# Performance work log

Hardware: AMD Instinct MI355X
Metric: run time of the kernel (lower is better)

Reference implementation:

```python
import jax, jax.numpy as jnp
import numpy as np
import math

B, N, C = 4096, 64, 128
H = 4
HD = C // H


def setup_inputs() -> dict:
    key = jax.random.key(0)
    ks = jax.random.split(key, 8)
    s = 1.0 / math.sqrt(C)
    return {
        "x": jax.random.normal(ks[0], (B, N, C), dtype=jnp.float32),
        "entropy_map": jax.random.uniform(ks[1], (B, 1, N), dtype=jnp.float32),
        "Wq": jax.random.normal(ks[2], (C, C), dtype=jnp.float32) * s,
        "bq": jnp.zeros((C,), dtype=jnp.float32),
        "Wk": jax.random.normal(ks[3], (C, C), dtype=jnp.float32) * s,
        "bk": jnp.zeros((C,), dtype=jnp.float32),
        "Wv": jax.random.normal(ks[4], (C, C), dtype=jnp.float32) * s,
        "bv": jnp.zeros((C,), dtype=jnp.float32),
        "Wo": jax.random.normal(ks[5], (C, C), dtype=jnp.float32) * s,
        "bo": jnp.zeros((C,), dtype=jnp.float32),
        "beta": 1,
    }


def reference(x, entropy_map, Wq, bq, Wk, bk, Wv, bv, Wo, bo, beta):
    b, n, c = x.shape
    # torch Linear: y = x @ W^T + b
    def proj(w, bias):
        y = jnp.einsum("bnc,dc->bnd", x, w) + bias
        return y.reshape(b, n, H, HD).transpose(0, 2, 1, 3)  # (B,H,N,HD)

    Q = proj(Wq, bq)
    K = proj(Wk, bk)
    V = proj(Wv, bv)
    scale = 1.0 / math.sqrt(HD)
    scores = jnp.einsum("bhnd,bhmd->bhnm", Q, K) * scale  # (B,H,N,N)
    attn = jax.nn.softmax(scores, axis=-1)
    # entropy gating: (B,1,N) -> (B,1,1,N), scales key columns then renormalizes
    gating = jnp.exp(-beta * entropy_map)[:, None, :, :]
    attn = attn * gating
    attn = attn / (attn.sum(axis=-1, keepdims=True) + 1e-9)
    out = jnp.einsum("bhnm,bhmd->bhnd", attn, V)  # (B,H,N,HD)
    out = out.transpose(0, 2, 1, 3).reshape(b, n, c)
    return jnp.einsum("bnc,dc->bnd", out, Wo) + bo
```

## Files before the change

### kernel.cpp

```cpp
#include <hip/hip_runtime.h>
#include <hip/hip_bf16.h>

#define NTOK 64
#define CDIM 128

typedef __attribute__((ext_vector_type(4))) float  f32x4;
typedef __attribute__((ext_vector_type(8))) short  bf16x8;
typedef __attribute__((ext_vector_type(4))) short  s16x4;

__device__ __forceinline__ short f2bf(float f) {
  unsigned u = __float_as_uint(f);
  unsigned r = (u + 0x7fffu + ((u >> 16) & 1u)) >> 16;
  return (short)r;
}

__device__ __forceinline__ int swz(int row, int cb, int stride) {
  return row * stride + (cb ^ ((row & 7) << 4));
}

__global__ void wconv_kernel(const float* __restrict__ wq, const float* __restrict__ wk,
                             const float* __restrict__ wv, const float* __restrict__ wo,
                             short* __restrict__ wbf) {
  int t = blockIdx.x * 256 + threadIdx.x;
  wbf[t]         = f2bf(wq[t]);
  wbf[16384 + t] = f2bf(wk[t]);
  wbf[32768 + t] = f2bf(wv[t]);
  wbf[49152 + t] = f2bf(wo[t]);
}

#define XO_OFF   0
#define Q_OFF    16384
#define K_OFF    32768
#define P_OFF    16384
#define VT_OFF   49152
#define GATE_OFF 65536
#define SMEM_BYTES (65536 + 256)

__global__ __launch_bounds__(256, 2) void fused_attn(
    const float* __restrict__ x, const float* __restrict__ ent,
    const short* __restrict__ wbf,
    const float* __restrict__ bq, const float* __restrict__ bk,
    const float* __restrict__ bv, const float* __restrict__ bo,
    const int* __restrict__ beta, float* __restrict__ out)
{
  __shared__ unsigned char sm[SMEM_BYTES];
  float* gate = (float*)(sm + GATE_OFF);
  const int tid  = threadIdx.x;
  const int lane = tid & 63;
  const int w    = tid >> 6;
  const int g    = lane >> 4;
  const int li   = lane & 15;
  const int b    = blockIdx.x;

  {
    const float* xb = x + (size_t)b * (NTOK * CDIM);
    #pragma unroll
    for (int it = 0; it < 8; ++it) {
      int f = (tid + 256 * it) * 4;
      int row = f >> 7, col = f & 127;
      float4 v = *reinterpret_cast<const float4*>(xb + f);
      s16x4 pk;
      pk.x = f2bf(v.x); pk.y = f2bf(v.y); pk.z = f2bf(v.z); pk.w = f2bf(v.w);
      *reinterpret_cast<s16x4*>(sm + XO_OFF + swz(row, col * 2, 256)) = pk;
    }
    if (tid < NTOK) {
      float bf = (float)beta[0];
      gate[tid] = -bf * ent[(size_t)b * NTOK + tid];
    }
  }
  __syncthreads();

  bf16x8 xf[4][4];
  #pragma unroll
  for (int ti = 0; ti < 4; ++ti) {
    #pragma unroll
    for (int kk = 0; kk < 4; ++kk) {
      int row = ti * 16 + li;
      int cb  = (kk * 32 + g * 8) * 2;
      xf[ti][kk] = *reinterpret_cast<const bf16x8*>(sm + XO_OFF + swz(row, cb, 256));
    }
  }

  const f32x4 zero4 = {0.f, 0.f, 0.f, 0.f};

  {
    const short* wmat = wbf + ((w < 2) ? 0 : 16384);
    const float* bias = (w < 2) ? bq : bk;
    const int dbase   = (w & 1) * 64;
    const int qkbase  = (w < 2) ? Q_OFF : K_OFF;

    f32x4 acc[4][4];
    #pragma unroll
    for (int mi = 0; mi < 4; ++mi)
      #pragma unroll
      for (int ni = 0; ni < 4; ++ni) acc[mi][ni] = zero4;

    #pragma unroll
    for (int mi = 0; mi < 4; ++mi) {
      bf16x8 af[4];
      #pragma unroll
      for (int kk = 0; kk < 4; ++kk)
        af[kk] = *reinterpret_cast<const bf16x8*>(wmat + (dbase + mi * 16 + li) * CDIM + kk * 32 + g * 8);
      #pragma unroll
      for (int ni = 0; ni < 4; ++ni)
        #pragma unroll
        for (int kk = 0; kk < 4; ++kk)
          acc[mi][ni] = __builtin_amdgcn_mfma_f32_16x16x32_bf16(af[kk], xf[ni][kk], acc[mi][ni], 0, 0, 0);
    }
    #pragma unroll
    for (int mi = 0; mi < 4; ++mi) {
      int d0 = dbase + mi * 16 + g * 4;
      float b0 = bias[d0 + 0], b1 = bias[d0 + 1], b2 = bias[d0 + 2], b3 = bias[d0 + 3];
      #pragma unroll
      for (int ni = 0; ni < 4; ++ni) {
        int row = ni * 16 + li;
        int cb  = d0 * 2;
        s16x4 pk;
        pk.x = f2bf(acc[mi][ni].x + b0);
        pk.y = f2bf(acc[mi][ni].y + b1);
        pk.z = f2bf(acc[mi][ni].z + b2);
        pk.w = f2bf(acc[mi][ni].w + b3);
        *reinterpret_cast<s16x4*>(sm + qkbase + swz(row, cb, 256)) = pk;
      }
    }
  }

  {
    const short* wv_ = wbf + 32768;
    f32x4 accv[4][2];
    #pragma unroll
    for (int mi = 0; mi < 4; ++mi) { accv[mi][0] = zero4; accv[mi][1] = zero4; }
    bf16x8 bfv[2][4];
    #pragma unroll
    for (int n2 = 0; n2 < 2; ++n2)
      #pragma unroll
      for (int kk = 0; kk < 4; ++kk)
        bfv[n2][kk] = *reinterpret_cast<const bf16x8*>(wv_ + (w * 32 + n2 * 16 + li) * CDIM + kk * 32 + g * 8);
    #pragma unroll
    for (int mi = 0; mi < 4; ++mi)
      #pragma unroll
      for (int n2 = 0; n2 < 2; ++n2)
        #pragma unroll
        for (int kk = 0; kk < 4; ++kk)
          accv[mi][n2] = __builtin_amdgcn_mfma_f32_16x16x32_bf16(xf[mi][kk], bfv[n2][kk], accv[mi][n2], 0, 0, 0);
    #pragma unroll
    for (int mi = 0; mi < 4; ++mi) {
      #pragma unroll
      for (int n2 = 0; n2 < 2; ++n2) {
        int d = w * 32 + n2 * 16 + li;
        float bb = bv[d];
        int cb = (mi * 16 + g * 4) * 2;
        s16x4 pk;
        pk.x = f2bf(accv[mi][n2].x + bb);
        pk.y = f2bf(accv[mi][n2].y + bb);
        pk.z = f2bf(accv[mi][n2].z + bb);
        pk.w = f2bf(accv[mi][n2].w + bb);
        *reinterpret_cast<s16x4*>(sm + VT_OFF + swz(d, cb, 128)) = pk;
      }
    }
  }
  __syncthreads();

  const float scale = 0.17677669529663688f;
  f32x4 st[4][4];
  {
    bf16x8 kf[4], qf[4];
    int cb = (w * 32 + g * 8) * 2;
    #pragma unroll
    for (int t = 0; t < 4; ++t) {
      int row = t * 16 + li;
      kf[t] = *reinterpret_cast<const bf16x8*>(sm + K_OFF + swz(row, cb, 256));
      qf[t] = *reinterpret_cast<const bf16x8*>(sm + Q_OFF + swz(row, cb, 256));
    }
    #pragma unroll
    for (int mj = 0; mj < 4; ++mj)
      #pragma unroll
      for (int ni = 0; ni < 4; ++ni)
        st[mj][ni] = __builtin_amdgcn_mfma_f32_16x16x32_bf16(kf[mj], qf[ni], zero4, 0, 0, 0);
  }
  float gv[16];
  #pragma unroll
  for (int mj = 0; mj < 4; ++mj)
    #pragma unroll
    for (int r = 0; r < 4; ++r)
      gv[mj * 4 + r] = gate[mj * 16 + g * 4 + r];

  #pragma unroll
  for (int ni = 0; ni < 4; ++ni) {
    float mx = -3.0e38f;
    #pragma unroll
    for (int mj = 0; mj < 4; ++mj) {
      f32x4 v = st[mj][ni];
      v.x = v.x * scale + gv[mj * 4 + 0];
      v.y = v.y * scale + gv[mj * 4 + 1];
      v.z = v.z * scale + gv[mj * 4 + 2];
      v.w = v.w * scale + gv[mj * 4 + 3];
      st[mj][ni] = v;
      mx = fmaxf(mx, fmaxf(fmaxf(v.x, v.y), fmaxf(v.z, v.w)));
    }
    mx = fmaxf(mx, __shfl_xor(mx, 16));
    mx = fmaxf(mx, __shfl_xor(mx, 32));
    float sum = 0.f;
    #pragma unroll
    for (int mj = 0; mj < 4; ++mj) {
      f32x4 v = st[mj][ni];
      v.x = __expf(v.x - mx); v.y = __expf(v.y - mx);
      v.z = __expf(v.z - mx); v.w = __expf(v.w - mx);
      st[mj][ni] = v;
      sum += v.x + v.y + v.z + v.w;
    }
    sum += __shfl_xor(sum, 16);
    sum += __shfl_xor(sum, 32);
    float inv = 1.f / (sum + 1e-9f);
    #pragma unroll
    for (int mj = 0; mj < 4; ++mj) {
      st[mj][ni].x *= inv; st[mj][ni].y *= inv;
      st[mj][ni].z *= inv; st[mj][ni].w *= inv;
    }
  }
  __syncthreads();

  const int pb = P_OFF + w * 8192;
  #pragma unroll
  for (int mj = 0; mj < 4; ++mj) {
    int cb = (mj * 16 + g * 4) * 2;
    #pragma unroll
    for (int ni = 0; ni < 4; ++ni) {
      int row = ni * 16 + li;
      s16x4 pk;
      pk.x = f2bf(st[mj][ni].x); pk.y = f2bf(st[mj][ni].y);
      pk.z = f2bf(st[mj][ni].z); pk.w = f2bf(st[mj][ni].w);
      *reinterpret_cast<s16x4*>(sm + pb + swz(row, cb, 128)) = pk;
    }
  }

  {
    f32x4 accO[2][4];
    #pragma unroll
    for (int md = 0; md < 2; ++md)
      #pragma unroll
      for (int ni = 0; ni < 4; ++ni) accO[md][ni] = zero4;
    bf16x8 vf[2][2];
    #pragma unroll
    for (int md = 0; md < 2; ++md)
      #pragma unroll
      for (int ks = 0; ks < 2; ++ks) {
        int row = w * 32 + md * 16 + li;
        int cb  = (ks * 32 + g * 8) * 2;
        vf[md][ks] = *reinterpret_cast<const bf16x8*>(sm + VT_OFF + swz(row, cb, 128));
      }
    bf16x8 pf[4][2];
    #pragma unroll
    for (int ni = 0; ni < 4; ++ni)
      #pragma unroll
      for (int ks = 0; ks < 2; ++ks) {
        int row = ni * 16 + li;
        int cb  = (ks * 32 + g * 8) * 2;
        pf[ni][ks] = *reinterpret_cast<const bf16x8*>(sm + pb + swz(row, cb, 128));
      }
    #pragma unroll
    for (int md = 0; md < 2; ++md)
      #pragma unroll
      for (int ni = 0; ni < 4; ++ni)
        #pragma unroll
        for (int ks = 0; ks < 2; ++ks)
          accO[md][ni] = __builtin_amdgcn_mfma_f32_16x16x32_bf16(vf[md][ks], pf[ni][ks], accO[md][ni], 0, 0, 0);
    #pragma unroll
    for (int md = 0; md < 2; ++md) {
      int cb = (w * 32 + md * 16 + g * 4) * 2;
      #pragma unroll
      for (int ni = 0; ni < 4; ++ni) {
        int row = ni * 16 + li;
        s16x4 pk;
        pk.x = f2bf(accO[md][ni].x); pk.y = f2bf(accO[md][ni].y);
        pk.z = f2bf(accO[md][ni].z); pk.w = f2bf(accO[md][ni].w);
        *reinterpret_cast<s16x4*>(sm + XO_OFF + swz(row, cb, 256)) = pk;
      }
    }
  }
  __syncthreads();

  {
    const short* wo_ = wbf + 49152;
    f32x4 accY[4][2];
    #pragma unroll
    for (int mi = 0; mi < 4; ++mi) { accY[mi][0] = zero4; accY[mi][1] = zero4; }
    bf16x8 of[4][4];
    #pragma unroll
    for (int mi = 0; mi < 4; ++mi)
      #pragma unroll
      for (int kk = 0; kk < 4; ++kk) {
        int row = mi * 16 + li;
        int cb  = (kk * 32 + g * 8) * 2;
        of[mi][kk] = *reinterpret_cast<const bf16x8*>(sm + XO_OFF + swz(row, cb, 256));
      }
    bf16x8 wf[2][4];
    #pragma unroll
    for (int n2 = 0; n2 < 2; ++n2)
      #pragma unroll
      for (int kk = 0; kk < 4; ++kk)
        wf[n2][kk] = *reinterpret_cast<const bf16x8*>(wo_ + (w * 32 + n2 * 16 + li) * CDIM + kk * 32 + g * 8);
    #pragma unroll
    for (int mi = 0; mi < 4; ++mi)
      #pragma unroll
      for (int n2 = 0; n2 < 2; ++n2)
        #pragma unroll
        for (int kk = 0; kk < 4; ++kk)
          accY[mi][n2] = __builtin_amdgcn_mfma_f32_16x16x32_bf16(of[mi][kk], wf[n2][kk], accY[mi][n2], 0, 0, 0);
    float* yb = out + (size_t)b * (NTOK * CDIM);
    #pragma unroll
    for (int n2 = 0; n2 < 2; ++n2) {
      int dout = w * 32 + n2 * 16 + li;
      float bb = bo[dout];
      #pragma unroll
      for (int mi = 0; mi < 4; ++mi) {
        int i0 = mi * 16 + g * 4;
        yb[(i0 + 0) * CDIM + dout] = accY[mi][n2].x + bb;
        yb[(i0 + 1) * CDIM + dout] = accY[mi][n2].y + bb;
        yb[(i0 + 2) * CDIM + dout] = accY[mi][n2].z + bb;
        yb[(i0 + 3) * CDIM + dout] = accY[mi][n2].w + bb;
      }
    }
  }
}

extern "C" void kernel_launch(void* const* d_in, const int* in_sizes, int n_in,
                              void* d_out, int out_size, void* d_ws, size_t ws_size,
                              hipStream_t stream) {
  const float* x    = (const float*)d_in[0];
  const float* ent  = (const float*)d_in[1];
  const float* wq   = (const float*)d_in[2];
  const float* bq   = (const float*)d_in[3];
  const float* wk   = (const float*)d_in[4];
  const float* bk   = (const float*)d_in[5];
  const float* wv   = (const float*)d_in[6];
  const float* bv   = (const float*)d_in[7];
  const float* wo   = (const float*)d_in[8];
  const float* bo   = (const float*)d_in[9];
  const int*   beta = (const int*)d_in[10];

  short* wbf = (short*)d_ws;
  const int B = in_sizes[0] / (NTOK * CDIM);

  wconv_kernel<<<64, 256, 0, stream>>>(wq, wk, wv, wo, wbf);
  fused_attn<<<B, 256, 0, stream>>>(x, ent, wbf, bq, bk, bv, bo, beta, (float*)d_out);
}
```

Measured before the change: 108.1 us.

## Shrink shared memory to 48KB for three blocks per CU and vectorize output stores

Reorders the projections so V is computed before Q/K, which lets Q overwrite the x buffer and the P and attention-output buffers reuse the freed regions. Shared memory drops from 64KB to 48KB, and launch bounds are raised to three blocks per CU to increase occupancy. It also swaps operands in the output projection so each thread writes contiguous float4 values, replaces the manual bf16 rounding with packed conversion intrinsics, and vectorizes the weight conversion kernel. The extra barriers needed for buffer reuse and the tighter register budget could offset the occupancy gain.

```diff
diff --git a/kernel.cpp b/kernel.cpp
--- a/kernel.cpp
+++ b/kernel.cpp
@@ -8,10 +8,11 @@
 typedef __attribute__((ext_vector_type(8))) short  bf16x8;
 typedef __attribute__((ext_vector_type(4))) short  s16x4;
 
-__device__ __forceinline__ short f2bf(float f) {
-  unsigned u = __float_as_uint(f);
-  unsigned r = (u + 0x7fffu + ((u >> 16) & 1u)) >> 16;
-  return (short)r;
+__device__ __forceinline__ s16x4 pk4(f32x4 v) {
+  union { __hip_bfloat162 h[2]; s16x4 s; } u;
+  u.h[0] = __float22bfloat162_rn(float2{v.x, v.y});
+  u.h[1] = __float22bfloat162_rn(float2{v.z, v.w});
+  return u.s;
 }
 
 __device__ __forceinline__ int swz(int row, int cb, int stride) {
@@ -21,22 +22,24 @@
 __global__ void wconv_kernel(const float* __restrict__ wq, const float* __restrict__ wk,
                              const float* __restrict__ wv, const float* __restrict__ wo,
                              short* __restrict__ wbf) {
-  int t = blockIdx.x * 256 + threadIdx.x;
-  wbf[t]         = f2bf(wq[t]);
-  wbf[16384 + t] = f2bf(wk[t]);
-  wbf[32768 + t] = f2bf(wv[t]);
-  wbf[49152 + t] = f2bf(wo[t]);
-}
-
-#define XO_OFF   0
-#define Q_OFF    16384
-#define K_OFF    32768
-#define P_OFF    16384
-#define VT_OFF   49152
-#define GATE_OFF 65536
-#define SMEM_BYTES (65536 + 256)
-
-__global__ __launch_bounds__(256, 2) void fused_attn(
+  int t = (blockIdx.x * 256 + threadIdx.x) * 4;
+  f32x4 a = *reinterpret_cast<const f32x4*>(wq + t);
+  f32x4 b = *reinterpret_cast<const f32x4*>(wk + t);
+  f32x4 c = *reinterpret_cast<const f32x4*>(wv + t);
+  f32x4 d = *reinterpret_cast<const f32x4*>(wo + t);
+  *reinterpret_cast<s16x4*>(wbf + t)         = pk4(a);
+  *reinterpret_cast<s16x4*>(wbf + 16384 + t) = pk4(b);
+  *reinterpret_cast<s16x4*>(wbf + 32768 + t) = pk4(c);
+  *reinterpret_cast<s16x4*>(wbf + 49152 + t) = pk4(d);
+}
+
+#define A_OFF    0
+#define B_OFF    16384
+#define C_OFF    32768
+#define GATE_OFF 49152
+#define SMEM_BYTES (49152 + 256)
+
+__global__ __launch_bounds__(256, 3) void fused_attn(
     const float* __restrict__ x, const float* __restrict__ ent,
     const short* __restrict__ wbf,
     const float* __restrict__ bq, const float* __restrict__ bk,
@@ -58,72 +61,23 @@
     for (int it = 0; it < 8; ++it) {
       int f = (tid + 256 * it) * 4;
       int row = f >> 7, col = f & 127;
-      float4 v = *reinterpret_cast<const float4*>(xb + f);
-      s16x4 pk;
-      pk.x = f2bf(v.x); pk.y = f2bf(v.y); pk.z = f2bf(v.z); pk.w = f2bf(v.w);
-      *reinterpret_cast<s16x4*>(sm + XO_OFF + swz(row, col * 2, 256)) = pk;
-    }
-    if (tid < NTOK) {
-      float bf = (float)beta[0];
-      gate[tid] = -bf * ent[(size_t)b * NTOK + tid];
-    }
+      f32x4 v = *reinterpret_cast<const f32x4*>(xb + f);
+      *reinterpret_cast<s16x4*>(sm + A_OFF + swz(row, col * 2, 256)) = pk4(v);
+    }
+    if (tid < NTOK) gate[tid] = -(float)beta[0] * ent[(size_t)b * NTOK + tid];
   }
   __syncthreads();
 
   bf16x8 xf[4][4];
   #pragma unroll
-  for (int ti = 0; ti < 4; ++ti) {
-    #pragma unroll
-    for (int kk = 0; kk < 4; ++kk) {
-      int row = ti * 16 + li;
-      int cb  = (kk * 32 + g * 8) * 2;
-      xf[ti][kk] = *reinterpret_cast<const bf16x8*>(sm + XO_OFF + swz(row, cb, 256));
-    }
-  }
+  for (int ti = 0; ti < 4; ++ti)
+    #pragma unroll
+    for (int kk = 0; kk < 4; ++kk)
+      xf[ti][kk] = *reinterpret_cast<const bf16x8*>(sm + A_OFF + swz(ti * 16 + li, (kk * 32 + g * 8) * 2, 256));
+
+  __syncthreads();
 
   const f32x4 zero4 = {0.f, 0.f, 0.f, 0.f};
-
-  {
-    const short* wmat = wbf + ((w < 2) ? 0 : 16384);
-    const float* bias = (w < 2) ? bq : bk;
-    const int dbase   = (w & 1) * 64;
-    const int qkbase  = (w < 2) ? Q_OFF : K_OFF;
-
-    f32x4 acc[4][4];
-    #pragma unroll
-    for (int mi = 0; mi < 4; ++mi)
-      #pragma unroll
-      for (int ni = 0; ni < 4; ++ni) acc[mi][ni] = zero4;
-
-    #pragma unroll
-    for (int mi = 0; mi < 4; ++mi) {
-      bf16x8 af[4];
-      #pragma unroll
-      for (int kk = 0; kk < 4; ++kk)
-        af[kk] = *reinterpret_cast<const bf16x8*>(wmat + (dbase + mi * 16 + li) * CDIM + kk * 32 + g * 8);
-      #pragma unroll
-      for (int ni = 0; ni < 4; ++ni)
-        #pragma unroll
-        for (int kk = 0; kk < 4; ++kk)
-          acc[mi][ni] = __builtin_amdgcn_mfma_f32_16x16x32_bf16(af[kk], xf[ni][kk], acc[mi][ni], 0, 0, 0);
-    }
-    #pragma unroll
-    for (int mi = 0; mi < 4; ++mi) {
-      int d0 = dbase + mi * 16 + g * 4;
-      float b0 = bias[d0 + 0], b1 = bias[d0 + 1], b2 = bias[d0 + 2], b3 = bias[d0 + 3];
-      #pragma unroll
-      for (int ni = 0; ni < 4; ++ni) {
-        int row = ni * 16 + li;
-        int cb  = d0 * 2;
-        s16x4 pk;
-        pk.x = f2bf(acc[mi][ni].x + b0);
-        pk.y = f2bf(acc[mi][ni].y + b1);
-        pk.z = f2bf(acc[mi][ni].z + b2);
-        pk.w = f2bf(acc[mi][ni].w + b3);
-        *reinterpret_cast<s16x4*>(sm + qkbase + swz(row, cb, 256)) = pk;
-      }
-    }
-  }
 
   {
     const short* wv_ = wbf + 32768;
@@ -144,18 +98,44 @@
         for (int kk = 0; kk < 4; ++kk)
           accv[mi][n2] = __builtin_amdgcn_mfma_f32_16x16x32_bf16(xf[mi][kk], bfv[n2][kk], accv[mi][n2], 0, 0, 0);
     #pragma unroll
-    for (int mi = 0; mi < 4; ++mi) {
+    for (int mi = 0; mi < 4; ++mi)
       #pragma unroll
       for (int n2 = 0; n2 < 2; ++n2) {
         int d = w * 32 + n2 * 16 + li;
         float bb = bv[d];
-        int cb = (mi * 16 + g * 4) * 2;
-        s16x4 pk;
-        pk.x = f2bf(accv[mi][n2].x + bb);
-        pk.y = f2bf(accv[mi][n2].y + bb);
-        pk.z = f2bf(accv[mi][n2].z + bb);
-        pk.w = f2bf(accv[mi][n2].w + bb);
-        *reinterpret_cast<s16x4*>(sm + VT_OFF + swz(d, cb, 128)) = pk;
+        f32x4 v = accv[mi][n2];
+        v.x += bb; v.y += bb; v.z += bb; v.w += bb;
+        *reinterpret_cast<s16x4*>(sm + C_OFF + swz(d, (mi * 16 + g * 4) * 2, 128)) = pk4(v);
+      }
+  }
+
+  {
+    const short* wmat = wbf + ((w < 2) ? 0 : 16384);
+    const float* bias = (w < 2) ? bq : bk;
+    const int dbase   = (w & 1) * 64;
+    const int qkoff   = (w < 2) ? A_OFF : B_OFF;
+
+    #pragma unroll
+    for (int mi = 0; mi < 4; ++mi) {
+      bf16x8 af[4];
+      #pragma unroll
+      for (int kk = 0; kk < 4; ++kk)
+        af[kk] = *reinterpret_cast<const bf16x8*>(wmat + (dbase + mi * 16 + li) * CDIM + kk * 32 + g * 8);
+      f32x4 acc[4];
+      #pragma unroll
+      for (int ni = 0; ni < 4; ++ni) acc[ni] = zero4;
+      #pragma unroll
+      for (int ni = 0; ni < 4; ++ni)
+        #pragma unroll
+        for (int kk = 0; kk < 4; ++kk)
+          acc[ni] = __builtin_amdgcn_mfma_f32_16x16x32_bf16(af[kk], xf[ni][kk], acc[ni], 0, 0, 0);
+      int d0 = dbase + mi * 16 + g * 4;
+      float4 b4 = *reinterpret_cast<const float4*>(bias + d0);
+      #pragma unroll
+      for (int ni = 0; ni < 4; ++ni) {
+        f32x4 v = acc[ni];
+        v.x += b4.x; v.y += b4.y; v.z += b4.z; v.w += b4.w;
+        *reinterpret_cast<s16x4*>(sm + qkoff + swz(ni * 16 + li, d0 * 2, 256)) = pk4(v);
       }
     }
   }
@@ -168,9 +148,8 @@
     int cb = (w * 32 + g * 8) * 2;
     #pragma unroll
     for (int t = 0; t < 4; ++t) {
-      int row = t * 16 + li;
-      kf[t] = *reinterpret_cast<const bf16x8*>(sm + K_OFF + swz(row, cb, 256));
-      qf[t] = *reinterpret_cast<const bf16x8*>(sm + Q_OFF + swz(row, cb, 256));
+      kf[t] = *reinterpret_cast<const bf16x8*>(sm + B_OFF + swz(t * 16 + li, cb, 256));
+      qf[t] = *reinterpret_cast<const bf16x8*>(sm + A_OFF + swz(t * 16 + li, cb, 256));
     }
     #pragma unroll
     for (int mj = 0; mj < 4; ++mj)
@@ -220,18 +199,13 @@
   }
   __syncthreads();
 
-  const int pb = P_OFF + w * 8192;
+  unsigned char* pb = sm + w * 8192;
   #pragma unroll
   for (int mj = 0; mj < 4; ++mj) {
     int cb = (mj * 16 + g * 4) * 2;
     #pragma unroll
-    for (int ni = 0; ni < 4; ++ni) {
-      int row = ni * 16 + li;
-      s16x4 pk;
-      pk.x = f2bf(st[mj][ni].x); pk.y = f2bf(st[mj][ni].y);
-      pk.z = f2bf(st[mj][ni].z); pk.w = f2bf(st[mj][ni].w);
-      *reinterpret_cast<s16x4*>(sm + pb + swz(row, cb, 128)) = pk;
-    }
+    for (int ni = 0; ni < 4; ++ni)
+      *reinterpret_cast<s16x4*>(pb + swz(ni * 16 + li, cb, 128)) = pk4(st[mj][ni]);
   }
 
   {
@@ -244,20 +218,14 @@
     #pragma unroll
     for (int md = 0; md < 2; ++md)
       #pragma unroll
-      for (int ks = 0; ks < 2; ++ks) {
-        int row = w * 32 + md * 16 + li;
-        int cb  = (ks * 32 + g * 8) * 2;
-        vf[md][ks] = *reinterpret_cast<const bf16x8*>(sm + VT_OFF + swz(row, cb, 128));
-      }
+      for (int ks = 0; ks < 2; ++ks)
+        vf[md][ks] = *reinterpret_cast<const bf16x8*>(sm + C_OFF + swz(w * 32 + md * 16 + li, (ks * 32 + g * 8) * 2, 128));
     bf16x8 pf[4][2];
     #pragma unroll
     for (int ni = 0; ni < 4; ++ni)
       #pragma unroll
-      for (int ks = 0; ks < 2; ++ks) {
-        int row = ni * 16 + li;
-        int cb  = (ks * 32 + g * 8) * 2;
-        pf[ni][ks] = *reinterpret_cast<const bf16x8*>(sm + pb + swz(row, cb, 128));
-      }
+      for (int ks = 0; ks < 2; ++ks)
+        pf[ni][ks] = *reinterpret_cast<const bf16x8*>(pb + swz(ni * 16 + li, (ks * 32 + g * 8) * 2, 128));
     #pragma unroll
     for (int md = 0; md < 2; ++md)
       #pragma unroll
@@ -265,60 +233,54 @@
         #pragma unroll
         for (int ks = 0; ks < 2; ++ks)
           accO[md][ni] = __builtin_amdgcn_mfma_f32_16x16x32_bf16(vf[md][ks], pf[ni][ks], accO[md][ni], 0, 0, 0);
+    __syncthreads();
     #pragma unroll
     for (int md = 0; md < 2; ++md) {
       int cb = (w * 32 + md * 16 + g * 4) * 2;
       #pragma unroll
-      for (int ni = 0; ni < 4; ++ni) {
-        int row = ni * 16 + li;
-        s16x4 pk;
-        pk.x = f2bf(accO[md][ni].x); pk.y = f2bf(accO[md][ni].y);
-        pk.z = f2bf(accO[md][ni].z); pk.w = f2bf(accO[md][ni].w);
-        *reinterpret_cast<s16x4*>(sm + XO_OFF + swz(row, cb, 256)) = pk;
-      }
+      for (int ni = 0; ni < 4; ++ni)
+        *reinterpret_cast<s16x4*>(sm + C_OFF + swz(ni * 16 + li, cb, 256)) = pk4(accO[md][ni]);
     }
   }
   __syncthreads();
 
   {
     const short* wo_ = wbf + 49152;
-    f32x4 accY[4][2];
-    #pragma unroll
-    for (int mi = 0; mi < 4; ++mi) { accY[mi][0] = zero4; accY[mi][1] = zero4; }
+    f32x4 accY[2][4];
+    #pragma unroll
+    for (int mi = 0; mi < 2; ++mi)
+      #pragma unroll
+      for (int ni = 0; ni < 4; ++ni) accY[mi][ni] = zero4;
+    bf16x8 wfa[2][4];
+    #pragma unroll
+    for (int mi = 0; mi < 2; ++mi)
+      #pragma unroll
+      for (int kk = 0; kk < 4; ++kk)
+        wfa[mi][kk] = *reinterpret_cast<const bf16x8*>(wo_ + (w * 32 + mi * 16 + li) * CDIM + kk * 32 + g * 8);
     bf16x8 of[4][4];
     #pragma unroll
-    for (int mi = 0; mi < 4; ++mi)
-      #pragma unroll
-      for (int kk = 0; kk < 4; ++kk) {
-        int row = mi * 16 + li;
-        int cb  = (kk * 32 + g * 8) * 2;
-        of[mi][kk] = *reinterpret_cast<const bf16x8*>(sm + XO_OFF + swz(row, cb, 256));
-      }
-    bf16x8 wf[2][4];
-    #pragma unroll
-    for (int n2 = 0; n2 < 2; ++n2)
+    for (int ni = 0; ni < 4; ++ni)
       #pragma unroll
       for (int kk = 0; kk < 4; ++kk)
-        wf[n2][kk] = *reinterpret_cast<const bf16x8*>(wo_ + (w * 32 + n2 * 16 + li) * CDIM + kk * 32 + g * 8);
-    #pragma unroll
-    for (int mi = 0; mi < 4; ++mi)
-      #pragma unroll
-      for (int n2 = 0; n2 < 2; ++n2)
+        of[ni][kk] = *reinterpret_cast<const bf16x8*>(sm + C_OFF + swz(ni * 16 + li, (kk * 32 + g * 8) * 2, 256));
+    #pragma unroll
+    for (int mi = 0; mi < 2; ++mi)
+      #pragma unroll
+      for (int ni = 0; ni < 4; ++ni)
         #pragma unroll
         for (int kk = 0; kk < 4; ++kk)
-          accY[mi][n2] = __builtin_amdgcn_mfma_f32_16x16x32_bf16(of[mi][kk], wf[n2][kk], accY[mi][n2], 0, 0, 0);
+          accY[mi][ni] = __builtin_amdgcn_mfma_f32_16x16x32_bf16(wfa[mi][kk], of[ni][kk], accY[mi][ni], 0, 0, 0);
     float* yb = out + (size_t)b * (NTOK * CDIM);
     #pragma unroll
-    for (int n2 = 0; n2 < 2; ++n2) {
-      int dout = w * 32 + n2 * 16 + li;
-      float bb = bo[dout];
-      #pragma unroll
-      for (int mi = 0; mi < 4; ++mi) {
-        int i0 = mi * 16 + g * 4;
-        yb[(i0 + 0) * CDIM + dout] = accY[mi][n2].x + bb;
-        yb[(i0 + 1) * CDIM + dout] = accY[mi][n2].y + bb;
-        yb[(i0 + 2) * CDIM + dout] = accY[mi][n2].z + bb;
-        yb[(i0 + 3) * CDIM + dout] = accY[mi][n2].w + bb;
+    for (int mi = 0; mi < 2; ++mi) {
+      int dout0 = w * 32 + mi * 16 + g * 4;
+      float4 bo4 = *reinterpret_cast<const float4*>(bo + dout0);
+      #pragma unroll
+      for (int ni = 0; ni < 4; ++ni) {
+        int i = ni * 16 + li;
+        f32x4 y = accY[mi][ni];
+        y.x += bo4.x; y.y += bo4.y; y.z += bo4.z; y.w += bo4.w;
+        *reinterpret_cast<f32x4*>(yb + i * CDIM + dout0) = y;
       }
     }
   }
@@ -342,6 +304,6 @@
   short* wbf = (short*)d_ws;
   const int B = in_sizes[0] / (NTOK * CDIM);
 
-  wconv_kernel<<<64, 256, 0, stream>>>(wq, wk, wv, wo, wbf);
+  wconv_kernel<<<16, 256, 0, stream>>>(wq, wk, wv, wo, wbf);
   fused_attn<<<B, 256, 0, stream>>>(x, ent, wbf, bq, bk, bv, bo, beta, (float*)d_out);
 }
```

Result: faster. 99.86 us (-7.7%).
